# Kernel optimization log

Measured on AMD Instinct MI355X. Metric: run time of the kernel, lower is better.

## Reference

```python
import jax, jax.numpy as jnp
import numpy as np
from jax import lax

H = 128

def _lstm_gates(x, h, c, w_ih, w_hh, b_ih, b_hh):
    # PyTorch gate order: i, f, g, o
    g = x @ w_ih.T + h @ w_hh.T + b_ih + b_hh
    i, f, gg, o = jnp.split(g, 4, axis=-1)
    c_new = jax.nn.sigmoid(f) * c + jax.nn.sigmoid(i) * jnp.tanh(gg)
    h_new = jax.nn.sigmoid(o) * jnp.tanh(c_new)
    return h_new, c_new

def _lstm_layer(x_btF, w_ih, w_hh, b_ih, b_hh):
    B = x_btF.shape[0]
    h0 = jnp.zeros((B, H), x_btF.dtype)
    c0 = jnp.zeros((B, H), x_btF.dtype)
    def step(carry, xt):
        h, c = carry
        h, c = _lstm_gates(xt, h, c, w_ih, w_hh, b_ih, b_hh)
        return (h, c), h
    (h_T, c_T), ys = lax.scan(step, (h0, c0), jnp.swapaxes(x_btF, 0, 1))
    return jnp.swapaxes(ys, 0, 1), h_T, c_T

def setup_inputs() -> dict:
    key = jax.random.key(0)
    ks = jax.random.split(key, 20)
    B, T, D, P = 4096, 200, 2, 3
    s = 1.0 / np.sqrt(H)
    u = lambda k, shp: jax.random.uniform(k, shp, jnp.float32, -s, s)
    return {
        'x_hist': jax.random.normal(ks[0], (B, T, D), jnp.float32),
        'params': jax.random.normal(ks[1], (B, P), jnp.float32),
        'pred_len': 200,
        'w_ih0': u(ks[2], (4 * H, D)), 'w_hh0': u(ks[3], (4 * H, H)),
        'b_ih0': u(ks[4], (4 * H,)), 'b_hh0': u(ks[5], (4 * H,)),
        'w_ih1': u(ks[6], (4 * H, H)), 'w_hh1': u(ks[7], (4 * H, H)),
        'b_ih1': u(ks[8], (4 * H,)), 'b_hh1': u(ks[9], (4 * H,)),
        'dec_w_ih': u(ks[10], (4 * H, D + P)), 'dec_w_hh': u(ks[11], (4 * H, H)),
        'dec_b_ih': u(ks[12], (4 * H,)), 'dec_b_hh': u(ks[13], (4 * H,)),
        'proj_w': u(ks[14], (H, P)), 'proj_b': u(ks[15], (H,)),
        'out_w': u(ks[16], (2, H)), 'out_b': u(ks[17], (2,)),
    }

def reference(x_hist, params, pred_len, w_ih0, w_hh0, b_ih0, b_hh0,
              w_ih1, w_hh1, b_ih1, b_hh1, dec_w_ih, dec_w_hh, dec_b_ih,
              dec_b_hh, proj_w, proj_b, out_w, out_b):
    # 2-layer encoder LSTM; only last layer's final (h, c) are used
    y1, _, _ = _lstm_layer(x_hist, w_ih0, w_hh0, b_ih0, b_hh0)
    _, h_n, c_n = _lstm_layer(y1, w_ih1, w_hh1, b_ih1, b_hh1)
    h = h_n + params @ proj_w.T + proj_b
    c = c_n
    cur = x_hist[:, -1, :]
    def step(carry, _):
        h, c, cur = carry
        inp = jnp.concatenate([cur, params], axis=-1)
        h, c = _lstm_gates(inp, h, c, dec_w_ih, dec_w_hh, dec_b_ih, dec_b_hh)
        cur = h @ out_w.T + out_b
        return (h, c, cur), cur
    _, preds = lax.scan(step, (h, c, cur), None, length=pred_len)
    return jnp.swapaxes(preds, 0, 1)  # [B, pred_len, 2]
```

## Files before the change

kernel.cpp:

```cpp
#include <hip/hip_runtime.h>
#include <stdint.h>

typedef __bf16 bf16x8 __attribute__((ext_vector_type(8)));
typedef float  f32x4  __attribute__((ext_vector_type(4)));

#define PRED   200
#define TSTEPS 200
#define NBLK   256

#define ASTR   280
#define ALO    136
#define ABUFE  (16*ASTR*2)
#define W_BYTES 131072
#define A_OFF   W_BYTES
#define LDS_A   (A_OFF + 2*ABUFE)
#define STG_OFF (A_OFF + 2*ABUFE)
#define LDS_C   (STG_OFF + ABUFE)

#define ABUFD  8192
#define LDS_D  (2*ABUFD)

#define STATE_FLOATS ((size_t)NBLK*4*2048)

__device__ __forceinline__ float sigm(float x){ return 1.0f/(1.0f+__expf(-x)); }
__device__ __forceinline__ float tanhx(float x){
  float t=__expf(-2.0f*fabsf(x)); float y=(1.0f-t)/(1.0f+t); return copysignf(y,x);
}
__device__ __forceinline__ bf16x8 hi8(float4 a, float4 b){
  bf16x8 r; r[0]=(__bf16)a.x; r[1]=(__bf16)a.y; r[2]=(__bf16)a.z; r[3]=(__bf16)a.w;
  r[4]=(__bf16)b.x; r[5]=(__bf16)b.y; r[6]=(__bf16)b.z; r[7]=(__bf16)b.w; return r;
}
__device__ __forceinline__ bf16x8 lo8(float4 a, float4 b, bf16x8 h){
  bf16x8 r;
  r[0]=(__bf16)(a.x-(float)h[0]); r[1]=(__bf16)(a.y-(float)h[1]);
  r[2]=(__bf16)(a.z-(float)h[2]); r[3]=(__bf16)(a.w-(float)h[3]);
  r[4]=(__bf16)(b.x-(float)h[4]); r[5]=(__bf16)(b.y-(float)h[5]);
  r[6]=(__bf16)(b.z-(float)h[6]); r[7]=(__bf16)(b.w-(float)h[7]); return r;
}
#define MFMA(A,B,C) __builtin_amdgcn_mfma_f32_16x16x32_bf16((A),(B),(C),0,0,0)

__device__ __forceinline__ int aoff(int row, int col){
  return row*512 + ((((col>>3) ^ (row&7)) << 4) | ((col&7)<<1));
}
__device__ __forceinline__ int frdoff(int c, int qd, int kt, int plane){
  return c*512 + (((((kt<<2)+qd) ^ (c&7)) | (plane<<4)) << 4);
}

__global__ void __launch_bounds__(512,2)
k_l0(const float* __restrict__ xh, const float* __restrict__ wih0,
     const float* __restrict__ whh0, const float* __restrict__ bih0,
     const float* __restrict__ bhh0, float* __restrict__ wsf,
     int chunkStart, int chunkLen, unsigned long long stageFloats)
{
  extern __shared__ char smem[];
  const int tid=threadIdx.x, wv=tid>>6, l=tid&63, c=l&15, qd=l>>4;
  const int hc=wv*16+c, blk=blockIdx.x, r0=blk*16;
  float* stf = wsf + stageFloats;
  #pragma unroll
  for (int i=0;i<16;++i){
    int f=i*8+wv, ntg=f>>2, kt=f&3;
    int g=(ntg&3)*128+(ntg>>2)*16+c, k=kt*32+qd*8;
    const float* s=whh0+g*128+k;
    *(bf16x8*)(smem+f*1024+l*16)=hi8(*(const float4*)s,*(const float4*)(s+4));
  }
  bf16x8 wlo[16];
  #pragma unroll
  for (int tt=0;tt<4;++tt)
    #pragma unroll
    for (int kt=0;kt<4;++kt){
      const float* s=whh0+(size_t)(tt*128+hc)*128+kt*32+qd*8;
      float4 a=*(const float4*)s, b=*(const float4*)(s+4);
      wlo[tt*4+kt]=lo8(a,b,hi8(a,b));
    }
  float b0[4], w0x[4], w0y[4];
  #pragma unroll
  for (int tt=0;tt<4;++tt){
    int g=tt*128+hc;
    b0[tt]=bih0[g]+bhh0[g]; w0x[tt]=wih0[2*g]; w0y[tt]=wih0[2*g+1];
  }
  float c0[4];
  {
    __bf16* B1=(__bf16*)(smem+A_OFF+ABUFE);
    const float* hst=stf+(size_t)(blk*4+0)*2048;
    const float* cst=stf+(size_t)(blk*4+1)*2048;
    #pragma unroll
    for (int i=0;i<4;++i){
      int e=tid*4+i, row=e>>7, col=e&127;
      float v=0.f; if(chunkStart) v=hst[e];
      __bf16 h=(__bf16)v;
      B1[row*ASTR+col]=h; B1[row*ASTR+ALO+col]=(__bf16)(v-(float)h);
    }
    #pragma unroll
    for (int j=0;j<4;++j){ float v=0.f; if(chunkStart) v=cst[(qd*4+j)*128+hc]; c0[j]=v; }
  }
  __syncthreads();
  for (int t=0;t<chunkLen;++t){
    const int p=t&1, tg=chunkStart+t;
    float2 xv[4];
    #pragma unroll
    for (int j=0;j<4;++j) xv[j]=*(const float2*)(xh+(size_t)(r0+qd*4+j)*400+tg*2);
    f32x4 acc[4];
    #pragma unroll
    for (int tt=0;tt<4;++tt) acc[tt]=(f32x4){b0[tt],b0[tt],b0[tt],b0[tt]};
    const char* Ar=smem+A_OFF+(size_t)(1-p)*ABUFE;
    #pragma unroll
    for (int kt=0;kt<4;++kt){
      bf16x8 ah=*(const bf16x8*)(Ar+(c*ASTR+kt*32+qd*8)*2);
      bf16x8 al=*(const bf16x8*)(Ar+(c*ASTR+ALO+kt*32+qd*8)*2);
      #pragma unroll
      for (int tt=0;tt<4;++tt){
        bf16x8 bh=*(const bf16x8*)(smem+(size_t)((wv*4+tt)*4+kt)*1024+l*16);
        acc[tt]=MFMA(ah,bh,acc[tt]);
        acc[tt]=MFMA(al,bh,acc[tt]);
        acc[tt]=MFMA(ah,wlo[tt*4+kt],acc[tt]);
      }
    }
    __bf16* Aw=(__bf16*)(smem+A_OFF+(size_t)p*ABUFE);
    float* h0o=wsf+((size_t)t*NBLK+blk)*2048;
    #pragma unroll
    for (int j=0;j<4;++j){
      float gi=acc[0][j]+xv[j].x*w0x[0]+xv[j].y*w0y[0];
      float gf=acc[1][j]+xv[j].x*w0x[1]+xv[j].y*w0y[1];
      float gg=acc[2][j]+xv[j].x*w0x[2]+xv[j].y*w0y[2];
      float go=acc[3][j]+xv[j].x*w0x[3]+xv[j].y*w0y[3];
      float cn=sigm(gf)*c0[j]+sigm(gi)*tanhx(gg); c0[j]=cn;
      float hn=sigm(go)*tanhx(cn);
      int row=qd*4+j;
      __bf16 hh=(__bf16)hn;
      Aw[row*ASTR+hc]=hh; Aw[row*ASTR+ALO+hc]=(__bf16)(hn-(float)hh);
      h0o[row*128+hc]=hn;
      if (t==chunkLen-1){
        stf[(size_t)(blk*4+0)*2048+row*128+hc]=hn;
        stf[(size_t)(blk*4+1)*2048+row*128+hc]=cn;
      }
    }
    __syncthreads();
  }
}

__global__ void __launch_bounds__(512,2)
k_l1(const float* __restrict__ wih1, const float* __restrict__ whh1,
     const float* __restrict__ bih1, const float* __restrict__ bhh1,
     float* __restrict__ wsf, int chunkStart, int chunkLen,
     unsigned long long stageFloats)
{
  extern __shared__ char smem[];
  const int tid=threadIdx.x, wv=tid>>6, l=tid&63, c=l&15, qd=l>>4;
  const int hc=wv*16+c, blk=blockIdx.x;
  float* stf = wsf + stageFloats;
  #pragma unroll
  for (int i=0;i<16;++i){
    int f=i*8+wv, ntg=f>>2, kt=f&3;
    int g=(ntg&3)*128+(ntg>>2)*16+c, k=kt*32+qd*8;
    const float* s=wih1+g*128+k;
    *(bf16x8*)(smem+f*1024+l*16)=hi8(*(const float4*)s,*(const float4*)(s+4));
  }
  bf16x8 whh[16], whl[16];
  #pragma unroll
  for (int tt=0;tt<4;++tt)
    #pragma unroll
    for (int kt=0;kt<4;++kt){
      const float* s2=whh1+(size_t)(tt*128+hc)*128+kt*32+qd*8;
      float4 a2=*(const float4*)s2, b2=*(const float4*)(s2+4);
      bf16x8 h2=hi8(a2,b2);
      whh[tt*4+kt]=h2; whl[tt*4+kt]=lo8(a2,b2,h2);
    }
  float b1v[4];
  #pragma unroll
  for (int tt=0;tt<4;++tt){ int g=tt*128+hc; b1v[tt]=bih1[g]+bhh1[g]; }
  float c1[4];
  {
    __bf16* B1=(__bf16*)(smem+A_OFF+ABUFE);
    const float* hst=stf+(size_t)(blk*4+2)*2048;
    const float* cst=stf+(size_t)(blk*4+3)*2048;
    #pragma unroll
    for (int i=0;i<4;++i){
      int e=tid*4+i, row=e>>7, col=e&127;
      float v=0.f; if(chunkStart) v=hst[e];
      __bf16 h=(__bf16)v;
      B1[row*ASTR+col]=h; B1[row*ASTR+ALO+col]=(__bf16)(v-(float)h);
    }
    #pragma unroll
    for (int j=0;j<4;++j){ float v=0.f; if(chunkStart) v=cst[(qd*4+j)*128+hc]; c1[j]=v; }
  }
  float4 r4=*(const float4*)(wsf+((size_t)0*NBLK+blk)*2048+tid*4);
  __syncthreads();
  for (int t=0;t<chunkLen;++t){
    const int p=t&1;
    {
      __bf16* ST=(__bf16*)(smem+STG_OFF);
      int e=tid*4, row=e>>7, col=e&127;
      #pragma unroll
      for (int i=0;i<4;++i){
        float v=((const float*)&r4)[i]; __bf16 h=(__bf16)v;
        ST[row*ASTR+col+i]=h; ST[row*ASTR+ALO+col+i]=(__bf16)(v-(float)h);
      }
    }
    if (t+1<chunkLen) r4=*(const float4*)(wsf+((size_t)(t+1)*NBLK+blk)*2048+tid*4);
    __syncthreads();
    f32x4 acc[4];
    #pragma unroll
    for (int tt=0;tt<4;++tt) acc[tt]=(f32x4){b1v[tt],b1v[tt],b1v[tt],b1v[tt]};
    const char* Ar=smem+A_OFF+(size_t)(1-p)*ABUFE;
    const char* Sr=smem+STG_OFF;
    #pragma unroll
    for (int kt=0;kt<4;++kt){
      bf16x8 a0h=*(const bf16x8*)(Sr+(c*ASTR+kt*32+qd*8)*2);
      bf16x8 a0l=*(const bf16x8*)(Sr+(c*ASTR+ALO+kt*32+qd*8)*2);
      bf16x8 a1h=*(const bf16x8*)(Ar+(c*ASTR+kt*32+qd*8)*2);
      bf16x8 a1l=*(const bf16x8*)(Ar+(c*ASTR+ALO+kt*32+qd*8)*2);
      #pragma unroll
      for (int tt=0;tt<4;++tt){
        bf16x8 bh=*(const bf16x8*)(smem+(size_t)((wv*4+tt)*4+kt)*1024+l*16);
        const float* sw=wih1+(size_t)(tt*128+hc)*128+kt*32+qd*8;
        float4 wa=*(const float4*)sw, wb=*(const float4*)(sw+4);
        bf16x8 wl=lo8(wa,wb,hi8(wa,wb));
        acc[tt]=MFMA(a0h,bh,acc[tt]);
        acc[tt]=MFMA(a0l,bh,acc[tt]);
        acc[tt]=MFMA(a0h,wl,acc[tt]);
        acc[tt]=MFMA(a1h,whh[tt*4+kt],acc[tt]);
        acc[tt]=MFMA(a1l,whh[tt*4+kt],acc[tt]);
        acc[tt]=MFMA(a1h,whl[tt*4+kt],acc[tt]);
      }
    }
    __bf16* Aw=(__bf16*)(smem+A_OFF+(size_t)p*ABUFE);
    #pragma unroll
    for (int j=0;j<4;++j){
      float cn=sigm(acc[1][j])*c1[j]+sigm(acc[0][j])*tanhx(acc[2][j]); c1[j]=cn;
      float hn=sigm(acc[3][j])*tanhx(cn);
      int row=qd*4+j;
      __bf16 hh=(__bf16)hn;
      Aw[row*ASTR+hc]=hh; Aw[row*ASTR+ALO+hc]=(__bf16)(hn-(float)hh);
      if (t==chunkLen-1){
        stf[(size_t)(blk*4+2)*2048+row*128+hc]=hn;
        stf[(size_t)(blk*4+3)*2048+row*128+hc]=cn;
      }
    }
    __syncthreads();
  }
}

__global__ void __launch_bounds__(512,1)
k_dec(const float* __restrict__ xh, const float* __restrict__ pprm,
      const float* __restrict__ dwihp, const float* __restrict__ dwhh,
      const float* __restrict__ dbih, const float* __restrict__ dbhh,
      const float* __restrict__ pw, const float* __restrict__ pb,
      const float* __restrict__ ow, const float* __restrict__ ob,
      const float* __restrict__ wsf, float* __restrict__ out,
      unsigned long long stageFloats)
{
  extern __shared__ char smem[];
  const int tid=threadIdx.x, wv=tid>>6, l=tid&63, c=l&15, qd=l>>4;
  const int hc=wv*16+c, blk=blockIdx.x, r0=blk*16;
  const float* stf = wsf + stageFloats;
  float ob0=ob[0], ob1=ob[1];
  float prm[4][3];
  #pragma unroll
  for (int j=0;j<4;++j){
    size_t r=(size_t)(r0+qd*4+j);
    prm[j][0]=pprm[r*3+0]; prm[j][1]=pprm[r*3+1]; prm[j][2]=pprm[r*3+2];
  }
  float ptF[4][4], dw0[4], dw1[4];
  #pragma unroll
  for (int tt=0;tt<4;++tt){
    int g=tt*128+hc;
    float db=dbih[g]+dbhh[g];
    dw0[tt]=dwihp[g*5+0]; dw1[tt]=dwihp[g*5+1];
    #pragma unroll
    for (int j=0;j<4;++j)
      ptF[tt][j]=db+prm[j][0]*dwihp[g*5+2]+prm[j][1]*dwihp[g*5+3]+prm[j][2]*dwihp[g*5+4]
                 +dw0[tt]*ob0+dw1[tt]*ob1;
  }
  bf16x8 whi[16], wlo[16];
  #pragma unroll
  for (int tt=0;tt<4;++tt)
    #pragma unroll
    for (int kt=0;kt<4;++kt){
      int g=tt*128+hc, k=kt*32+qd*8;
      float4 a=*(const float4*)(dwhh+(size_t)g*128+k), b=*(const float4*)(dwhh+(size_t)g*128+k+4);
      float4 o0a=*(const float4*)(ow+k),     o0b=*(const float4*)(ow+k+4);
      float4 o1a=*(const float4*)(ow+128+k), o1b=*(const float4*)(ow+128+k+4);
      a.x+=dw0[tt]*o0a.x+dw1[tt]*o1a.x; a.y+=dw0[tt]*o0a.y+dw1[tt]*o1a.y;
      a.z+=dw0[tt]*o0a.z+dw1[tt]*o1a.z; a.w+=dw0[tt]*o0a.w+dw1[tt]*o1a.w;
      b.x+=dw0[tt]*o0b.x+dw1[tt]*o1b.x; b.y+=dw0[tt]*o0b.y+dw1[tt]*o1b.y;
      b.z+=dw0[tt]*o0b.z+dw1[tt]*o1b.z; b.w+=dw0[tt]*o0b.w+dw1[tt]*o1b.w;
      whi[tt*4+kt]=hi8(a,b); wlo[tt*4+kt]=lo8(a,b,whi[tt*4+kt]);
    }
  bf16x8 owh[4], owl[4];
  #pragma unroll
  for (int kt=0;kt<4;++kt){
    int cc=(c<2)?c:0;
    const float* s=ow+cc*128+kt*32+qd*8;
    float4 a=*(const float4*)s, b=*(const float4*)(s+4);
    if (c>=2){ a=(float4){0,0,0,0}; b=(float4){0,0,0,0}; }
    owh[kt]=hi8(a,b); owl[kt]=lo8(a,b,owh[kt]);
  }
  const float* h1s=stf+(size_t)(blk*4+2)*2048;
  const float* c1s=stf+(size_t)(blk*4+3)*2048;
  float c1[4], cx0[4], cx1[4];
  {
    float prj0=pw[hc*3+0], prj1=pw[hc*3+1], prj2=pw[hc*3+2], prjb=pb[hc];
    char* B0=smem;
    #pragma unroll
    for (int j=0;j<4;++j){
      int row=qd*4+j;
      float hd=h1s[row*128+hc]+prm[j][0]*prj0+prm[j][1]*prj1+prm[j][2]*prj2+prjb;
      __bf16 h=(__bf16)hd;
      *(__bf16*)(B0+aoff(row,hc))=h;
      *(__bf16*)(B0+aoff(row,hc+128))=(__bf16)(hd-(float)h);
      c1[j]=c1s[row*128+hc];
      float2 xx=*(const float2*)(xh+(size_t)(r0+row)*400+398);
      cx0[j]=xx.x; cx1[j]=xx.y;
    }
  }
  __syncthreads();
  float corr0[4], corr1[4];
  {
    const char* Ar=smem;
    f32x4 pv={0.f,0.f,0.f,0.f};
    #pragma unroll
    for (int kt=0;kt<4;++kt){
      bf16x8 ah=*(const bf16x8*)(Ar+frdoff(c,qd,kt,0));
      bf16x8 al=*(const bf16x8*)(Ar+frdoff(c,qd,kt,1));
      pv=MFMA(ah,owh[kt],pv); pv=MFMA(al,owh[kt],pv); pv=MFMA(ah,owl[kt],pv);
    }
    #pragma unroll
    for (int j=0;j<4;++j){
      float p0=__shfl(pv[j], (l&48),   64);
      float p1=__shfl(pv[j], (l&48)|1, 64);
      corr0[j]=cx0[j]-(p0+ob0);
      corr1[j]=cx1[j]-(p1+ob1);
    }
  }
  for (int s=0;s<PRED;++s){
    const int q=s&1;
    const char* Ar=smem+(size_t)q*ABUFD;
    bf16x8 ah[4], al[4];
    #pragma unroll
    for (int kt=0;kt<4;++kt){
      ah[kt]=*(const bf16x8*)(Ar+frdoff(c,qd,kt,0));
      al[kt]=*(const bf16x8*)(Ar+frdoff(c,qd,kt,1));
    }
    f32x4 aA[4], aB[4];
    #pragma unroll
    for (int tt=0;tt<4;++tt){ aA[tt]=(f32x4){ptF[tt][0],ptF[tt][1],ptF[tt][2],ptF[tt][3]}; aB[tt]=(f32x4){0.f,0.f,0.f,0.f}; }
    #pragma unroll
    for (int kt=0;kt<4;++kt)
      #pragma unroll
      for (int tt=0;tt<4;++tt){
        f32x4* tgt=(kt<2)?&aA[tt]:&aB[tt];
        *tgt=MFMA(ah[kt],whi[tt*4+kt],*tgt);
        *tgt=MFMA(al[kt],whi[tt*4+kt],*tgt);
        *tgt=MFMA(ah[kt],wlo[tt*4+kt],*tgt);
      }
    f32x4 pv={0.f,0.f,0.f,0.f};
    if (wv==0){
      #pragma unroll
      for (int kt=0;kt<4;++kt){
        pv=MFMA(ah[kt],owh[kt],pv); pv=MFMA(al[kt],owh[kt],pv); pv=MFMA(ah[kt],owl[kt],pv);
      }
    }
    char* Aw=smem+(size_t)(1-q)*ABUFD;
    #pragma unroll
    for (int j=0;j<4;++j){
      float gi=aA[0][j]+aB[0][j];
      float gf=aA[1][j]+aB[1][j];
      float gg=aA[2][j]+aB[2][j];
      float go=aA[3][j]+aB[3][j];
      if (s==0){
        gi+=corr0[j]*dw0[0]+corr1[j]*dw1[0];
        gf+=corr0[j]*dw0[1]+corr1[j]*dw1[1];
        gg+=corr0[j]*dw0[2]+corr1[j]*dw1[2];
        go+=corr0[j]*dw0[3]+corr1[j]*dw1[3];
      }
      float cn=sigm(gf)*c1[j]+sigm(gi)*tanhx(gg); c1[j]=cn;
      float hn=sigm(go)*tanhx(cn);
      int row=qd*4+j;
      __bf16 hh=(__bf16)hn;
      *(__bf16*)(Aw+aoff(row,hc))=hh;
      *(__bf16*)(Aw+aoff(row,hc+128))=(__bf16)(hn-(float)hh);
    }
    if (s && wv==0 && c<2){
      float obv=c?ob1:ob0;
      #pragma unroll
      for (int j=0;j<4;++j)
        out[(size_t)(r0+qd*4+j)*400+(s-1)*2+c]=pv[j]+obv;
    }
    __syncthreads();
  }
  if (wv==0){
    const char* Ar=smem+(size_t)(PRED&1)*ABUFD;
    f32x4 pv={0.f,0.f,0.f,0.f};
    #pragma unroll
    for (int kt=0;kt<4;++kt){
      bf16x8 ah=*(const bf16x8*)(Ar+frdoff(c,qd,kt,0));
      bf16x8 al=*(const bf16x8*)(Ar+frdoff(c,qd,kt,1));
      pv=MFMA(ah,owh[kt],pv); pv=MFMA(al,owh[kt],pv); pv=MFMA(ah,owl[kt],pv);
    }
    if (c<2){
      float obv=c?ob1:ob0;
      #pragma unroll
      for (int j=0;j<4;++j)
        out[(size_t)(r0+qd*4+j)*400+(PRED-1)*2+c]=pv[j]+obv;
    }
  }
}

extern "C" void kernel_launch(void* const* d_in, const int* in_sizes, int n_in,
                              void* d_out, int out_size, void* d_ws, size_t ws_size,
                              hipStream_t stream)
{
  (void)out_size;
  const int base = (n_in >= 19 && in_sizes[2] == 1) ? 3 : 2;
  const float* xh   = (const float*)d_in[0];
  const float* prm  = (const float*)d_in[1];
  const float* wih0 = (const float*)d_in[base+0];
  const float* whh0 = (const float*)d_in[base+1];
  const float* bih0 = (const float*)d_in[base+2];
  const float* bhh0 = (const float*)d_in[base+3];
  const float* wih1 = (const float*)d_in[base+4];
  const float* whh1 = (const float*)d_in[base+5];
  const float* bih1 = (const float*)d_in[base+6];
  const float* bhh1 = (const float*)d_in[base+7];
  const float* dwih = (const float*)d_in[base+8];
  const float* dwhh = (const float*)d_in[base+9];
  const float* dbih = (const float*)d_in[base+10];
  const float* dbhh = (const float*)d_in[base+11];
  const float* pw   = (const float*)d_in[base+12];
  const float* pb   = (const float*)d_in[base+13];
  const float* ow   = (const float*)d_in[base+14];
  const float* ob   = (const float*)d_in[base+15];
  float* wsf = (float*)d_ws;

  size_t wsFloats = ws_size / 4;
  size_t avail = (wsFloats > STATE_FLOATS) ? (wsFloats - STATE_FLOATS) : 0;
  int chunkLen = (int)(avail / ((size_t)NBLK * 2048));
  if (chunkLen > 50) chunkLen = 50;
  if (chunkLen < 1)  chunkLen = 1;
  unsigned long long stageFloats = (unsigned long long)chunkLen * NBLK * 2048;

  hipFuncSetAttribute((const void*)k_l0, hipFuncAttributeMaxDynamicSharedMemorySize, LDS_A);
  hipFuncSetAttribute((const void*)k_l1, hipFuncAttributeMaxDynamicSharedMemorySize, LDS_C);

  for (int k0 = 0; k0 < TSTEPS; k0 += chunkLen){
    int len = chunkLen; if (k0 + len > TSTEPS) len = TSTEPS - k0;
    k_l0<<<NBLK,512,LDS_A,stream>>>(xh, wih0, whh0, bih0, bhh0, wsf, k0, len, stageFloats);
    k_l1<<<NBLK,512,LDS_C,stream>>>(wih1, whh1, bih1, bhh1, wsf, k0, len, stageFloats);
  }
  k_dec<<<NBLK,512,LDS_D,stream>>>(xh, prm, dwih, dwhh, dbih, dbhh,
                                   pw, pb, ow, ob, wsf, (float*)d_out, stageFloats);
}
```

Before: 1.905 ms.

## Defer global stores past barriers and keep Wih1 low-part in registers

In the layer-0 and decoder loops, the global writes of h and of predictions are delayed by one step and issued at the start of the next iteration, so they do not sit just before the barrier. In layer 1, the low-precision residual of Wih1 is precomputed once into 16 register vectors instead of being reloaded from global memory and converted every timestep. This removes redundant global loads and conversion work in the inner loop. The cost is higher register pressure, which may hurt occupancy under launch_bounds(512,2) or cause spills.

```diff
diff --git a/kernel.cpp b/kernel.cpp
--- a/kernel.cpp
+++ b/kernel.cpp
@@ -94,8 +94,14 @@
     for (int j=0;j<4;++j){ float v=0.f; if(chunkStart) v=cst[(qd*4+j)*128+hc]; c0[j]=v; }
   }
   __syncthreads();
+  float hprev[4];
   for (int t=0;t<chunkLen;++t){
     const int p=t&1, tg=chunkStart+t;
+    if (t){
+      float* h0p=wsf+((size_t)(t-1)*NBLK+blk)*2048;
+      #pragma unroll
+      for (int j=0;j<4;++j) h0p[(qd*4+j)*128+hc]=hprev[j];
+    }
     float2 xv[4];
     #pragma unroll
     for (int j=0;j<4;++j) xv[j]=*(const float2*)(xh+(size_t)(r0+qd*4+j)*400+tg*2);
@@ -116,7 +122,6 @@
       }
     }
     __bf16* Aw=(__bf16*)(smem+A_OFF+(size_t)p*ABUFE);
-    float* h0o=wsf+((size_t)t*NBLK+blk)*2048;
     #pragma unroll
     for (int j=0;j<4;++j){
       float gi=acc[0][j]+xv[j].x*w0x[0]+xv[j].y*w0y[0];
@@ -128,13 +133,19 @@
       int row=qd*4+j;
       __bf16 hh=(__bf16)hn;
       Aw[row*ASTR+hc]=hh; Aw[row*ASTR+ALO+hc]=(__bf16)(hn-(float)hh);
-      h0o[row*128+hc]=hn;
-      if (t==chunkLen-1){
-        stf[(size_t)(blk*4+0)*2048+row*128+hc]=hn;
-        stf[(size_t)(blk*4+1)*2048+row*128+hc]=cn;
-      }
+      hprev[j]=hn;
     }
     __syncthreads();
+  }
+  {
+    float* h0p=wsf+((size_t)(chunkLen-1)*NBLK+blk)*2048;
+    #pragma unroll
+    for (int j=0;j<4;++j){
+      int row=qd*4+j;
+      h0p[row*128+hc]=hprev[j];
+      stf[(size_t)(blk*4+0)*2048+row*128+hc]=hprev[j];
+      stf[(size_t)(blk*4+1)*2048+row*128+hc]=c0[j];
+    }
   }
 }
 
@@ -155,7 +166,7 @@
     const float* s=wih1+g*128+k;
     *(bf16x8*)(smem+f*1024+l*16)=hi8(*(const float4*)s,*(const float4*)(s+4));
   }
-  bf16x8 whh[16], whl[16];
+  bf16x8 whh[16], whl[16], wil[16];
   #pragma unroll
   for (int tt=0;tt<4;++tt)
     #pragma unroll
@@ -164,6 +175,9 @@
       float4 a2=*(const float4*)s2, b2=*(const float4*)(s2+4);
       bf16x8 h2=hi8(a2,b2);
       whh[tt*4+kt]=h2; whl[tt*4+kt]=lo8(a2,b2,h2);
+      const float* s3=wih1+(size_t)(tt*128+hc)*128+kt*32+qd*8;
+      float4 a3=*(const float4*)s3, b3=*(const float4*)(s3+4);
+      wil[tt*4+kt]=lo8(a3,b3,hi8(a3,b3));
     }
   float b1v[4];
   #pragma unroll
@@ -212,12 +226,9 @@
       #pragma unroll
       for (int tt=0;tt<4;++tt){
         bf16x8 bh=*(const bf16x8*)(smem+(size_t)((wv*4+tt)*4+kt)*1024+l*16);
-        const float* sw=wih1+(size_t)(tt*128+hc)*128+kt*32+qd*8;
-        float4 wa=*(const float4*)sw, wb=*(const float4*)(sw+4);
-        bf16x8 wl=lo8(wa,wb,hi8(wa,wb));
         acc[tt]=MFMA(a0h,bh,acc[tt]);
         acc[tt]=MFMA(a0l,bh,acc[tt]);
-        acc[tt]=MFMA(a0h,wl,acc[tt]);
+        acc[tt]=MFMA(a0h,wil[tt*4+kt],acc[tt]);
         acc[tt]=MFMA(a1h,whh[tt*4+kt],acc[tt]);
         acc[tt]=MFMA(a1l,whh[tt*4+kt],acc[tt]);
         acc[tt]=MFMA(a1h,whl[tt*4+kt],acc[tt]);
@@ -332,8 +343,15 @@
       corr1[j]=cx1[j]-(p1+ob1);
     }
   }
+  f32x4 pvPrev={0.f,0.f,0.f,0.f};
   for (int s=0;s<PRED;++s){
     const int q=s&1;
+    if (s>=2 && wv==0 && c<2){
+      float obv=c?ob1:ob0;
+      #pragma unroll
+      for (int j=0;j<4;++j)
+        out[(size_t)(r0+qd*4+j)*400+(s-2)*2+c]=pvPrev[j]+obv;
+    }
     const char* Ar=smem+(size_t)q*ABUFD;
     bf16x8 ah[4], al[4];
     #pragma unroll
@@ -380,13 +398,14 @@
       *(__bf16*)(Aw+aoff(row,hc))=hh;
       *(__bf16*)(Aw+aoff(row,hc+128))=(__bf16)(hn-(float)hh);
     }
-    if (s && wv==0 && c<2){
-      float obv=c?ob1:ob0;
-      #pragma unroll
-      for (int j=0;j<4;++j)
-        out[(size_t)(r0+qd*4+j)*400+(s-1)*2+c]=pv[j]+obv;
-    }
+    if (wv==0) pvPrev=pv;
     __syncthreads();
+  }
+  if (wv==0 && c<2){
+    float obv=c?ob1:ob0;
+    #pragma unroll
+    for (int j=0;j<4;++j)
+      out[(size_t)(r0+qd*4+j)*400+(PRED-2)*2+c]=pvPrev[j]+obv;
   }
   if (wv==0){
     const char* Ar=smem+(size_t)(PRED&1)*ABUFD;
```

Result: no change. 1.878 ms (-1.4%).
